# Performance work log

Measured on AMD Instinct MI355X. Metric: run time of the kernel, lower is better.

## Reference

```python
import jax, jax.numpy as jnp
import numpy as np

NEG_SLOPE = 0.2  # PyG GATConv default


def add_self_loops(edge_index, num_nodes):
    loops = jnp.arange(num_nodes, dtype=edge_index.dtype)
    return jnp.concatenate([edge_index, jnp.stack([loops, loops])], axis=1)


def gat_conv(x, edge_index, W, att_src, att_dst, bias, heads, out_ch, concat):
    # x: [N, F_in]; edge_index: [2, E] with row0=src(j), row1=dst(i)
    N = x.shape[0]
    xl = (x @ W).reshape(N, heads, out_ch)              # [N, H, C]
    src, dst = edge_index[0], edge_index[1]
    a_src = jnp.einsum('nhc,hc->nh', xl, att_src)        # [N, H]
    a_dst = jnp.einsum('nhc,hc->nh', xl, att_dst)        # [N, H]
    alpha = jax.nn.leaky_relu(a_src[src] + a_dst[dst], NEG_SLOPE)  # [E, H]
    # segment softmax over incoming edges of each dst node
    m = jax.ops.segment_max(alpha, dst, num_segments=N)  # [N, H]
    e = jnp.exp(alpha - m[dst])
    denom = jax.ops.segment_sum(e, dst, num_segments=N)
    coef = e / (denom[dst] + 1e-16)                      # [E, H]
    msg = xl[src] * coef[..., None]                      # [E, H, C]
    out = jax.ops.segment_sum(msg, dst, num_segments=N)  # [N, H, C]
    out = out.reshape(N, heads * out_ch) if concat else out.mean(axis=1)
    return out + bias


def setup_inputs() -> dict:
    key = jax.random.key(0)
    ks = jax.random.split(key, 12)
    N, E = 50000, 800000
    nfeat, nhid, nheads, nclass = 512, 8, 8, 16
    hid = nhid * nheads  # 64
    s1 = 1.0 / np.sqrt(nfeat)
    s2 = 1.0 / np.sqrt(hid)
    return {
        'x': jax.random.normal(ks[0], (N, nfeat), jnp.float32),
        'edge_index': jax.random.randint(ks[1], (2, E), 0, N, jnp.int64 if jax.config.jax_enable_x64 else jnp.int32),
        'W1': jax.random.uniform(ks[2], (nfeat, hid), jnp.float32, -s1, s1),
        'att_src1': jax.random.uniform(ks[3], (nheads, nhid), jnp.float32, -s2, s2),
        'att_dst1': jax.random.uniform(ks[4], (nheads, nhid), jnp.float32, -s2, s2),
        'bias1': jnp.zeros((hid,), jnp.float32),
        'W2': jax.random.uniform(ks[5], (hid, nclass), jnp.float32, -s2, s2),
        'att_src2': jax.random.uniform(ks[6], (1, nclass), jnp.float32, -0.25, 0.25),
        'att_dst2': jax.random.uniform(ks[7], (1, nclass), jnp.float32, -0.25, 0.25),
        'bias2': jnp.zeros((nclass,), jnp.float32),
    }


def reference(x, edge_index, W1, att_src1, att_dst1, bias1, W2, att_src2, att_dst2, bias2):
    N = x.shape[0]
    ei = add_self_loops(edge_index, N)
    # dropout layers are identity at inference
    h = gat_conv(x, ei, W1, att_src1, att_dst1, bias1, heads=8, out_ch=8, concat=True)
    o = gat_conv(h, ei, W2, att_src2, att_dst2, bias2, heads=1, out_ch=16, concat=True)
    o = jax.nn.elu(o)
    return jax.nn.log_softmax(o, axis=1)
```

## Files before the change

kernel.cpp:

```cpp
#include <hip/hip_runtime.h>
#include <hip/hip_bf16.h>
#include <math.h>

#define NEG_SLOPE 0.2f

typedef short short8 __attribute__((ext_vector_type(8)));
typedef float floatx4 __attribute__((ext_vector_type(4)));

static __device__ __forceinline__ float bf2f(unsigned short u) {
  return __uint_as_float(((unsigned int)u) << 16);
}
static __device__ __forceinline__ unsigned short f2bf(float f) {
  unsigned int u = __float_as_uint(f);
  u = (u + 0x7fffu + ((u >> 16) & 1u)) >> 16;
  return (unsigned short)u;
}
static __device__ __forceinline__ unsigned int pack2(float a, float b) {
  __hip_bfloat162 h = __float22bfloat162_rn(make_float2(a, b));
  unsigned int u;
  __builtin_memcpy(&u, &h, 4);
  return u;
}

__global__ void prep_kernel(const float* __restrict__ W1, unsigned short* __restrict__ W1t,
                            int* __restrict__ deg, const int* __restrict__ ei,
                            unsigned short* __restrict__ src16, unsigned short* __restrict__ dst16,
                            int N, int E) {
  int i = blockIdx.x * 256 + threadIdx.x;
  if (i < 32768) {
    int k = i >> 6, c = i & 63;
    W1t[c * 512 + k] = f2bf(W1[i]);
  }
  int j = i - 32768;
  if (j >= 0 && j < N) deg[j] = 1;
  int e = i - 32768 - N;
  if (e >= 0 && e < E) {
    src16[e] = (unsigned short)ei[e];
    dst16[e] = (unsigned short)ei[E + e];
  }
}

__global__ __launch_bounds__(256) void gemm1_mfma(const float* __restrict__ A,
                                                  const unsigned short* __restrict__ W1t,
                                                  const float* __restrict__ att_src,
                                                  const float* __restrict__ att_dst,
                                                  unsigned short* __restrict__ xlb,
                                                  float* __restrict__ a_src,
                                                  float* __restrict__ a_dst, int M) {
  __shared__ unsigned short As[64 * 72];
  __shared__ unsigned short Bs[64 * 72];
  int tid = threadIdx.x;
  int w = tid >> 6, lane = tid & 63;
  int q = lane >> 4, cl = lane & 15;
  int row0 = blockIdx.x << 6;
  floatx4 acc[4] = {};

  int sr = tid >> 2;
  int skq = (tid & 3) << 4;
  int arow = row0 + sr;
  const float* Aptr = A + (size_t)arow * 512 + skq;
  const unsigned short* Bptr = W1t + sr * 512 + skq;
  unsigned short* AsW = As + sr * 72 + skq;
  unsigned short* BsW = Bs + sr * 72 + skq;

  for (int k0 = 0; k0 < 512; k0 += 64) {
    float4 f0 = make_float4(0.f, 0.f, 0.f, 0.f), f1 = f0, f2 = f0, f3 = f0;
    if (arow < M) {
      f0 = *(const float4*)(Aptr + k0);
      f1 = *(const float4*)(Aptr + k0 + 4);
      f2 = *(const float4*)(Aptr + k0 + 8);
      f3 = *(const float4*)(Aptr + k0 + 12);
    }
    uint4 b0 = *(const uint4*)(Bptr + k0);
    uint4 b1 = *(const uint4*)(Bptr + k0 + 8);
    __syncthreads();
    uint4 a0, a1;
    a0.x = pack2(f0.x, f0.y); a0.y = pack2(f0.z, f0.w);
    a0.z = pack2(f1.x, f1.y); a0.w = pack2(f1.z, f1.w);
    a1.x = pack2(f2.x, f2.y); a1.y = pack2(f2.z, f2.w);
    a1.z = pack2(f3.x, f3.y); a1.w = pack2(f3.z, f3.w);
    *(uint4*)(AsW) = a0;
    *(uint4*)(AsW + 8) = a1;
    *(uint4*)(BsW) = b0;
    *(uint4*)(BsW + 8) = b1;
    __syncthreads();
#pragma unroll
    for (int kk = 0; kk < 2; ++kk) {
      short8 af = *(const short8*)(As + (w * 16 + cl) * 72 + kk * 32 + q * 8);
#pragma unroll
      for (int t = 0; t < 4; ++t) {
        short8 bf = *(const short8*)(Bs + (t * 16 + cl) * 72 + kk * 32 + q * 8);
        acc[t] = __builtin_amdgcn_mfma_f32_16x16x32_bf16(af, bf, acc[t], 0, 0, 0);
      }
    }
  }

  float asv[4], adv[4];
#pragma unroll
  for (int t = 0; t < 4; ++t) {
    asv[t] = att_src[t * 16 + cl];
    adv[t] = att_dst[t * 16 + cl];
  }
#pragma unroll
  for (int reg = 0; reg < 4; ++reg) {
    int r = row0 + w * 16 + q * 4 + reg;
    bool ok = r < M;
#pragma unroll
    for (int t = 0; t < 4; ++t) {
      float v = acc[t][reg];
      if (ok) xlb[(size_t)r * 64 + t * 16 + cl] = f2bf(v);
      float ps = v * asv[t];
      float pd = v * adv[t];
      ps += __shfl_xor(ps, 1); pd += __shfl_xor(pd, 1);
      ps += __shfl_xor(ps, 2); pd += __shfl_xor(pd, 2);
      ps += __shfl_xor(ps, 4); pd += __shfl_xor(pd, 4);
      if (ok && (cl & 7) == 0) {
        int h = t * 2 + (cl >> 3);
        a_src[r * 8 + h] = ps;
        a_dst[r * 8 + h] = pd;
      }
    }
  }
}

__global__ __launch_bounds__(256) void deg_hist_sliced(const unsigned short* __restrict__ dst16,
                                                       int* __restrict__ deg,
                                                       int E, int N, int ipc) {
  int slice = blockIdx.x & 7;
  int chunk = blockIdx.x >> 3;
  int lo = (int)(((long long)slice * N) >> 3);
  int hi = (int)(((long long)(slice + 1) * N) >> 3);
  int beg = chunk * ipc;
  int end = min(beg + ipc, E);
  for (int i = beg + threadIdx.x; i < end; i += 256) {
    int d = dst16[i];
    if (d >= lo && d < hi) atomicAdd(&deg[d], 1);
  }
}

__global__ __launch_bounds__(256) void partial_sums(const int* __restrict__ deg,
                                                    int* __restrict__ partials, int N) {
  __shared__ int ws[4];
  int base = blockIdx.x * 512;
  int tid = threadIdx.x;
  int i0 = base + tid * 2;
  int s = 0;
  if (i0 < N) s += deg[i0];
  if (i0 + 1 < N) s += deg[i0 + 1];
#pragma unroll
  for (int off = 32; off >= 1; off >>= 1) s += __shfl_xor(s, off, 64);
  if ((tid & 63) == 0) ws[tid >> 6] = s;
  __syncthreads();
  if (tid == 0) partials[blockIdx.x] = ws[0] + ws[1] + ws[2] + ws[3];
}

__global__ __launch_bounds__(256) void scan_partials(const int* __restrict__ partials,
                                                     int* __restrict__ blockoff,
                                                     int* __restrict__ rowptr, int nb, int N) {
  __shared__ int sums[256];
  int tid = threadIdx.x;
  int chunk = (nb + 255) >> 8;
  int start = tid * chunk, end = min(start + chunk, nb);
  int s = 0;
  for (int i = start; i < end; ++i) s += partials[i];
  sums[tid] = s;
  __syncthreads();
  for (int off = 1; off < 256; off <<= 1) {
    int t = (tid >= off) ? sums[tid - off] : 0;
    __syncthreads();
    sums[tid] += t;
    __syncthreads();
  }
  int run = (tid == 0) ? 0 : sums[tid - 1];
  for (int i = start; i < end; ++i) {
    blockoff[i] = run;
    run += partials[i];
  }
  if (tid == 255) rowptr[N] = sums[255];
}

__global__ __launch_bounds__(256) void scan_blocks(const int* __restrict__ deg,
                                                   const int* __restrict__ blockoff,
                                                   int* __restrict__ rowptr,
                                                   int* __restrict__ cursor, int N) {
  __shared__ int wavesum[4];
  int base = blockIdx.x * 512;
  int tid = threadIdx.x;
  int lane = tid & 63, wv = tid >> 6;
  int i0 = base + tid * 2;
  int d0 = (i0 < N) ? deg[i0] : 0;
  int d1 = (i0 + 1 < N) ? deg[i0 + 1] : 0;
  int s = d0 + d1;
  int v = s;
#pragma unroll
  for (int off = 1; off < 64; off <<= 1) {
    int t = __shfl_up(v, off, 64);
    if (lane >= off) v += t;
  }
  if (lane == 63) wavesum[wv] = v;
  __syncthreads();
  int woff = 0;
  for (int w = 0; w < wv; ++w) woff += wavesum[w];
  int excl = v - s + woff + blockoff[blockIdx.x];
  if (i0 < N) { rowptr[i0] = excl; cursor[i0] = excl; }
  if (i0 + 1 < N) { rowptr[i0 + 1] = excl + d0; cursor[i0 + 1] = excl + d0; }
}

__global__ __launch_bounds__(256) void scatter_sliced(const unsigned short* __restrict__ src16,
                                                      const unsigned short* __restrict__ dst16,
                                                      int* __restrict__ cursor,
                                                      unsigned short* __restrict__ srcs,
                                                      int E, int N, int ipc) {
  int slice = blockIdx.x & 7;
  int chunk = blockIdx.x >> 3;
  int lo = (int)(((long long)slice * N) >> 3);
  int hi = (int)(((long long)(slice + 1) * N) >> 3);
  int total = E + N;
  int beg = chunk * ipc;
  int end = min(beg + ipc, total);
  for (int i = beg + threadIdx.x; i < end; i += 256) {
    int d = (i < E) ? (int)dst16[i] : (i - E);
    if (d >= lo && d < hi) {
      int s = (i < E) ? (int)src16[i] : d;
      int pos = atomicAdd(&cursor[d], 1);
      srcs[pos] = (unsigned short)s;
    }
  }
}

__global__ __launch_bounds__(256) void agg1_csr(const int* __restrict__ rowptr,
                                                const unsigned short* __restrict__ srcs,
                                                const float* __restrict__ a_src,
                                                const float* __restrict__ a_dst,
                                                const unsigned short* __restrict__ xlb,
                                                float* __restrict__ agg1, int N) {
  int wave = (blockIdx.x * blockDim.x + threadIdx.x) >> 6;
  int lane = threadIdx.x & 63;
  if (wave >= N) return;
  int h = lane >> 3;
  int beg = rowptr[wave], end = rowptr[wave + 1];
  float ad = a_dst[wave * 8 + h];
  float den = 0.f, acc = 0.f;
  int p = beg;
  for (; p + 8 <= end; p += 8) {
    int myv = (int)srcs[p + (lane & 7)];
    int s0 = __builtin_amdgcn_readlane(myv, 0);
    int s1 = __builtin_amdgcn_readlane(myv, 1);
    int s2 = __builtin_amdgcn_readlane(myv, 2);
    int s3 = __builtin_amdgcn_readlane(myv, 3);
    int s4 = __builtin_amdgcn_readlane(myv, 4);
    int s5 = __builtin_amdgcn_readlane(myv, 5);
    int s6 = __builtin_amdgcn_readlane(myv, 6);
    int s7 = __builtin_amdgcn_readlane(myv, 7);
    float a0 = a_src[s0 * 8 + h], a1 = a_src[s1 * 8 + h];
    float a2 = a_src[s2 * 8 + h], a3 = a_src[s3 * 8 + h];
    float a4 = a_src[s4 * 8 + h], a5 = a_src[s5 * 8 + h];
    float a6 = a_src[s6 * 8 + h], a7 = a_src[s7 * 8 + h];
    float x0 = bf2f(xlb[(size_t)s0 * 64 + lane]);
    float x1 = bf2f(xlb[(size_t)s1 * 64 + lane]);
    float x2 = bf2f(xlb[(size_t)s2 * 64 + lane]);
    float x3 = bf2f(xlb[(size_t)s3 * 64 + lane]);
    float x4 = bf2f(xlb[(size_t)s4 * 64 + lane]);
    float x5 = bf2f(xlb[(size_t)s5 * 64 + lane]);
    float x6 = bf2f(xlb[(size_t)s6 * 64 + lane]);
    float x7 = bf2f(xlb[(size_t)s7 * 64 + lane]);
    a0 += ad; a1 += ad; a2 += ad; a3 += ad;
    a4 += ad; a5 += ad; a6 += ad; a7 += ad;
    a0 = a0 >= 0.f ? a0 : NEG_SLOPE * a0;
    a1 = a1 >= 0.f ? a1 : NEG_SLOPE * a1;
    a2 = a2 >= 0.f ? a2 : NEG_SLOPE * a2;
    a3 = a3 >= 0.f ? a3 : NEG_SLOPE * a3;
    a4 = a4 >= 0.f ? a4 : NEG_SLOPE * a4;
    a5 = a5 >= 0.f ? a5 : NEG_SLOPE * a5;
    a6 = a6 >= 0.f ? a6 : NEG_SLOPE * a6;
    a7 = a7 >= 0.f ? a7 : NEG_SLOPE * a7;
    float w0 = __expf(a0), w1 = __expf(a1), w2 = __expf(a2), w3 = __expf(a3);
    float w4 = __expf(a4), w5 = __expf(a5), w6 = __expf(a6), w7 = __expf(a7);
    den += ((w0 + w1) + (w2 + w3)) + ((w4 + w5) + (w6 + w7));
    acc += w0 * x0 + w1 * x1 + w2 * x2 + w3 * x3;
    acc += w4 * x4 + w5 * x5 + w6 * x6 + w7 * x7;
  }
  for (; p < end; ++p) {
    int s = __builtin_amdgcn_readfirstlane((int)srcs[p]);
    float a = a_src[s * 8 + h] + ad;
    a = a >= 0.f ? a : NEG_SLOPE * a;
    float w = __expf(a);
    den += w;
    acc += w * bf2f(xlb[(size_t)s * 64 + lane]);
  }
  agg1[(size_t)wave * 64 + lane] = acc / (den + 1e-16f);
}

__global__ __launch_bounds__(256) void gemm2_prep(const float* __restrict__ agg1,
                                                  const float* __restrict__ bias1,
                                                  const float* __restrict__ W2,
                                                  const float* __restrict__ att_src2,
                                                  const float* __restrict__ att_dst2,
                                                  float* __restrict__ xl2,
                                                  float* __restrict__ a_src2,
                                                  float* __restrict__ a_dst2, int N) {
  __shared__ float hs[16 * 68];
  int tid = threadIdx.x;
  int n0 = blockIdx.x << 4;
  {
    int node = tid >> 4;
    int off = (tid & 15) << 2;
    int nn = n0 + node;
    float4 v = make_float4(0.f, 0.f, 0.f, 0.f);
    if (nn < N) {
      v = *(const float4*)(agg1 + (size_t)nn * 64 + off);
      float4 b = *(const float4*)(bias1 + off);
      v.x += b.x; v.y += b.y; v.z += b.z; v.w += b.w;
    }
    *(float4*)(hs + node * 68 + off) = v;
  }
  __syncthreads();
  int t = tid >> 4, c = tid & 15;
  int n = n0 + t;
  if (n >= N) return;
  float sum = 0.f;
#pragma unroll
  for (int k = 0; k < 64; ++k) sum += hs[t * 68 + k] * W2[k * 16 + c];
  xl2[(size_t)n * 16 + c] = sum;
  float ps = sum * att_src2[c];
  float pd = sum * att_dst2[c];
#pragma unroll
  for (int w = 8; w >= 1; w >>= 1) {
    ps += __shfl_xor(ps, w, 16);
    pd += __shfl_xor(pd, w, 16);
  }
  if (c == 0) {
    a_src2[n] = ps;
    a_dst2[n] = pd;
  }
}

__global__ __launch_bounds__(256) void agg2_fin(const int* __restrict__ rowptr,
                                                const unsigned short* __restrict__ srcs,
                                                const float* __restrict__ a_src2,
                                                const float* __restrict__ a_dst2,
                                                const float* __restrict__ xl2,
                                                const float* __restrict__ bias2,
                                                float* __restrict__ out, int N) {
  int t = blockIdx.x * blockDim.x + threadIdx.x;
  int node = t >> 4;
  int c = t & 15;
  if (node >= N) return;
  int beg = rowptr[node], end = rowptr[node + 1];
  float ad = a_dst2[node];
  float den = 0.f, acc = 0.f;
  int p = beg;
  for (; p + 8 <= end; p += 8) {
    int s0 = srcs[p], s1 = srcs[p + 1], s2 = srcs[p + 2], s3 = srcs[p + 3];
    int s4 = srcs[p + 4], s5 = srcs[p + 5], s6 = srcs[p + 6], s7 = srcs[p + 7];
    float a0 = a_src2[s0], a1 = a_src2[s1], a2 = a_src2[s2], a3 = a_src2[s3];
    float a4 = a_src2[s4], a5 = a_src2[s5], a6 = a_src2[s6], a7 = a_src2[s7];
    float x0 = xl2[(size_t)s0 * 16 + c], x1 = xl2[(size_t)s1 * 16 + c];
    float x2 = xl2[(size_t)s2 * 16 + c], x3 = xl2[(size_t)s3 * 16 + c];
    float x4 = xl2[(size_t)s4 * 16 + c], x5 = xl2[(size_t)s5 * 16 + c];
    float x6 = xl2[(size_t)s6 * 16 + c], x7 = xl2[(size_t)s7 * 16 + c];
    a0 += ad; a1 += ad; a2 += ad; a3 += ad;
    a4 += ad; a5 += ad; a6 += ad; a7 += ad;
    a0 = a0 >= 0.f ? a0 : NEG_SLOPE * a0;
    a1 = a1 >= 0.f ? a1 : NEG_SLOPE * a1;
    a2 = a2 >= 0.f ? a2 : NEG_SLOPE * a2;
    a3 = a3 >= 0.f ? a3 : NEG_SLOPE * a3;
    a4 = a4 >= 0.f ? a4 : NEG_SLOPE * a4;
    a5 = a5 >= 0.f ? a5 : NEG_SLOPE * a5;
    a6 = a6 >= 0.f ? a6 : NEG_SLOPE * a6;
    a7 = a7 >= 0.f ? a7 : NEG_SLOPE * a7;
    float w0 = __expf(a0), w1 = __expf(a1), w2 = __expf(a2), w3 = __expf(a3);
    float w4 = __expf(a4), w5 = __expf(a5), w6 = __expf(a6), w7 = __expf(a7);
    den += ((w0 + w1) + (w2 + w3)) + ((w4 + w5) + (w6 + w7));
    acc += w0 * x0 + w1 * x1 + w2 * x2 + w3 * x3;
    acc += w4 * x4 + w5 * x5 + w6 * x6 + w7 * x7;
  }
  for (; p < end; ++p) {
    int s = srcs[p];
    float a = a_src2[s] + ad;
    a = a >= 0.f ? a : NEG_SLOPE * a;
    float w = __expf(a);
    den += w;
    acc += w * xl2[(size_t)s * 16 + c];
  }
  float o = acc / (den + 1e-16f) + bias2[c];
  o = o > 0.f ? o : expm1f(o);
  float mx = o;
#pragma unroll
  for (int w = 8; w >= 1; w >>= 1) mx = fmaxf(mx, __shfl_xor(mx, w, 16));
  float e = __expf(o - mx);
  float ssum = e;
#pragma unroll
  for (int w = 8; w >= 1; w >>= 1) ssum += __shfl_xor(ssum, w, 16);
  out[(size_t)node * 16 + c] = o - mx - logf(ssum);
}

extern "C" void kernel_launch(void* const* d_in, const int* in_sizes, int n_in,
                              void* d_out, int out_size, void* d_ws, size_t ws_size,
                              hipStream_t stream) {
  const float* x        = (const float*)d_in[0];
  const int*   ei       = (const int*)d_in[1];
  const float* W1       = (const float*)d_in[2];
  const float* att_src1 = (const float*)d_in[3];
  const float* att_dst1 = (const float*)d_in[4];
  const float* bias1    = (const float*)d_in[5];
  const float* W2       = (const float*)d_in[6];
  const float* att_src2 = (const float*)d_in[7];
  const float* att_dst2 = (const float*)d_in[8];
  const float* bias2    = (const float*)d_in[9];
  float* out = (float*)d_out;

  int N = in_sizes[0] / 512;
  int E = in_sizes[1] / 2;
  int nb = (N + 511) / 512;

  char* wsp = (char*)d_ws;
  auto alloc = [&](size_t bytes) {
    char* p = wsp;
    wsp += (bytes + 255) & ~(size_t)255;
    return p;
  };
  unsigned short* xlb   = (unsigned short*)alloc((size_t)N * 64 * 2);
  unsigned short* W1t   = (unsigned short*)alloc((size_t)512 * 64 * 2);
  float* a_src1 = (float*)alloc((size_t)N * 8 * 4);
  float* a_dst1 = (float*)alloc((size_t)N * 8 * 4);
  float* agg1   = (float*)alloc((size_t)N * 64 * 4);
  float* xl2    = (float*)alloc((size_t)N * 16 * 4);
  float* a_src2 = (float*)alloc((size_t)N * 4);
  float* a_dst2 = (float*)alloc((size_t)N * 4);
  int* deg      = (int*)alloc((size_t)N * 4);
  int* rowptr   = (int*)alloc((size_t)(N + 1) * 4);
  int* cursor   = (int*)alloc((size_t)N * 4);
  int* partials = (int*)alloc((size_t)nb * 4);
  int* blockoff = (int*)alloc((size_t)nb * 4);
  unsigned short* src16 = (unsigned short*)alloc((size_t)E * 2);
  unsigned short* dst16 = (unsigned short*)alloc((size_t)E * 2);
  unsigned short* srcs  = (unsigned short*)alloc((size_t)(E + N) * 2);

  const int NCHUNK = 256;
  int ipc_h = (E + NCHUNK - 1) / NCHUNK;
  int ipc_s = (E + N + NCHUNK - 1) / NCHUNK;

  prep_kernel<<<(32768 + N + E + 255) / 256, 256, 0, stream>>>(W1, W1t, deg, ei, src16, dst16, N, E);
  deg_hist_sliced<<<NCHUNK * 8, 256, 0, stream>>>(dst16, deg, E, N, ipc_h);
  partial_sums<<<nb, 256, 0, stream>>>(deg, partials, N);
  scan_partials<<<1, 256, 0, stream>>>(partials, blockoff, rowptr, nb, N);
  scan_blocks<<<nb, 256, 0, stream>>>(deg, blockoff, rowptr, cursor, N);
  scatter_sliced<<<NCHUNK * 8, 256, 0, stream>>>(src16, dst16, cursor, srcs, E, N, ipc_s);

  gemm1_mfma<<<(N + 63) / 64, 256, 0, stream>>>(x, W1t, att_src1, att_dst1,
                                                xlb, a_src1, a_dst1, N);
  agg1_csr<<<((size_t)N * 64 + 255) / 256, 256, 0, stream>>>(rowptr, srcs, a_src1, a_dst1,
                                                             xlb, agg1, N);
  gemm2_prep<<<(N + 15) / 16, 256, 0, stream>>>(agg1, bias1, W2, att_src2, att_dst2,
                                                xl2, a_src2, a_dst2, N);
  agg2_fin<<<((size_t)N * 16 + 255) / 256, 256, 0, stream>>>(rowptr, srcs, a_src2, a_dst2,
                                                             xl2, bias2, out, N);
}
```

Before: 331.1 us.

## Fuse degree histogram into GEMM1 launch and use single-pass chained scan

The degree histogram blocks are merged into the GEMM1 kernel launch as extra leading blocks, so histogram atomics run concurrently with the MFMA GEMM. The three-kernel scan (partial sums, partial scan, block scan) is replaced by one decoupled-lookback chained scan using per-block flags, which prep_kernel zeroes. This removes several kernel launches and lets the latency-bound histogram overlap the GEMM. The lookback relies on earlier blocks being scheduled first to avoid spinning.

```diff
diff --git a/kernel.cpp b/kernel.cpp
--- a/kernel.cpp
+++ b/kernel.cpp
@@ -25,7 +25,7 @@
 __global__ void prep_kernel(const float* __restrict__ W1, unsigned short* __restrict__ W1t,
                             int* __restrict__ deg, const int* __restrict__ ei,
                             unsigned short* __restrict__ src16, unsigned short* __restrict__ dst16,
-                            int N, int E) {
+                            int* __restrict__ flags, int nb, int N, int E) {
   int i = blockIdx.x * 256 + threadIdx.x;
   if (i < 32768) {
     int k = i >> 6, c = i & 63;
@@ -38,23 +38,41 @@
     src16[e] = (unsigned short)ei[e];
     dst16[e] = (unsigned short)ei[E + e];
   }
-}
-
-__global__ __launch_bounds__(256) void gemm1_mfma(const float* __restrict__ A,
+  int f = i - 32768 - N - E;
+  if (f >= 0 && f < nb) flags[f] = 0;
+}
+
+__global__ __launch_bounds__(256) void hist_gemm1(const int* __restrict__ ei,
+                                                  int* __restrict__ deg,
+                                                  const float* __restrict__ A,
                                                   const unsigned short* __restrict__ W1t,
                                                   const float* __restrict__ att_src,
                                                   const float* __restrict__ att_dst,
                                                   unsigned short* __restrict__ xlb,
                                                   float* __restrict__ a_src,
-                                                  float* __restrict__ a_dst, int M) {
+                                                  float* __restrict__ a_dst,
+                                                  int M, int E, int N, int ipc, int HB) {
   __shared__ unsigned short As[64 * 72];
   __shared__ unsigned short Bs[64 * 72];
+  if (blockIdx.x < (unsigned)HB) {
+    int slice = blockIdx.x & 7;
+    int chunk = blockIdx.x >> 3;
+    int lo = (int)(((long long)slice * N) >> 3);
+    int hi = (int)(((long long)(slice + 1) * N) >> 3);
+    int beg = chunk * ipc;
+    int end = min(beg + ipc, E);
+    for (int i = beg + threadIdx.x; i < end; i += 256) {
+      int d = ei[E + i];
+      if (d >= lo && d < hi) atomicAdd(&deg[d], 1);
+    }
+    return;
+  }
   int tid = threadIdx.x;
   int w = tid >> 6, lane = tid & 63;
   int q = lane >> 4, cl = lane & 15;
-  int row0 = blockIdx.x << 6;
+  int row0 = (blockIdx.x - HB) << 6;
+
   floatx4 acc[4] = {};
-
   int sr = tid >> 2;
   int skq = (tid & 3) << 4;
   int arow = row0 + sr;
@@ -123,68 +141,17 @@
   }
 }
 
-__global__ __launch_bounds__(256) void deg_hist_sliced(const unsigned short* __restrict__ dst16,
-                                                       int* __restrict__ deg,
-                                                       int E, int N, int ipc) {
-  int slice = blockIdx.x & 7;
-  int chunk = blockIdx.x >> 3;
-  int lo = (int)(((long long)slice * N) >> 3);
-  int hi = (int)(((long long)(slice + 1) * N) >> 3);
-  int beg = chunk * ipc;
-  int end = min(beg + ipc, E);
-  for (int i = beg + threadIdx.x; i < end; i += 256) {
-    int d = dst16[i];
-    if (d >= lo && d < hi) atomicAdd(&deg[d], 1);
-  }
-}
-
-__global__ __launch_bounds__(256) void partial_sums(const int* __restrict__ deg,
-                                                    int* __restrict__ partials, int N) {
-  __shared__ int ws[4];
-  int base = blockIdx.x * 512;
-  int tid = threadIdx.x;
-  int i0 = base + tid * 2;
-  int s = 0;
-  if (i0 < N) s += deg[i0];
-  if (i0 + 1 < N) s += deg[i0 + 1];
-#pragma unroll
-  for (int off = 32; off >= 1; off >>= 1) s += __shfl_xor(s, off, 64);
-  if ((tid & 63) == 0) ws[tid >> 6] = s;
-  __syncthreads();
-  if (tid == 0) partials[blockIdx.x] = ws[0] + ws[1] + ws[2] + ws[3];
-}
-
-__global__ __launch_bounds__(256) void scan_partials(const int* __restrict__ partials,
-                                                     int* __restrict__ blockoff,
-                                                     int* __restrict__ rowptr, int nb, int N) {
-  __shared__ int sums[256];
-  int tid = threadIdx.x;
-  int chunk = (nb + 255) >> 8;
-  int start = tid * chunk, end = min(start + chunk, nb);
-  int s = 0;
-  for (int i = start; i < end; ++i) s += partials[i];
-  sums[tid] = s;
-  __syncthreads();
-  for (int off = 1; off < 256; off <<= 1) {
-    int t = (tid >= off) ? sums[tid - off] : 0;
-    __syncthreads();
-    sums[tid] += t;
-    __syncthreads();
-  }
-  int run = (tid == 0) ? 0 : sums[tid - 1];
-  for (int i = start; i < end; ++i) {
-    blockoff[i] = run;
-    run += partials[i];
-  }
-  if (tid == 255) rowptr[N] = sums[255];
-}
-
-__global__ __launch_bounds__(256) void scan_blocks(const int* __restrict__ deg,
-                                                   const int* __restrict__ blockoff,
-                                                   int* __restrict__ rowptr,
-                                                   int* __restrict__ cursor, int N) {
+__global__ __launch_bounds__(256) void scan_chained(const int* __restrict__ deg,
+                                                    int* __restrict__ rowptr,
+                                                    int* __restrict__ cursor,
+                                                    int* __restrict__ block_agg,
+                                                    int* __restrict__ block_pfx,
+                                                    int* __restrict__ flags,
+                                                    int N, int nb) {
   __shared__ int wavesum[4];
-  int base = blockIdx.x * 512;
+  __shared__ int base_sh;
+  int bid = blockIdx.x;
+  int base = bid * 512;
   int tid = threadIdx.x;
   int lane = tid & 63, wv = tid >> 6;
   int i0 = base + tid * 2;
@@ -199,9 +166,32 @@
   }
   if (lane == 63) wavesum[wv] = v;
   __syncthreads();
-  int woff = 0;
+  int S = wavesum[0] + wavesum[1] + wavesum[2] + wavesum[3];
+  if (tid == 0) {
+    if (bid == 0) {
+      block_pfx[0] = S;
+      __hip_atomic_store(&flags[0], 2, __ATOMIC_RELEASE, __HIP_MEMORY_SCOPE_AGENT);
+      base_sh = 0;
+      if (nb == 1) rowptr[N] = S;
+    } else {
+      block_agg[bid] = S;
+      __hip_atomic_store(&flags[bid], 1, __ATOMIC_RELEASE, __HIP_MEMORY_SCOPE_AGENT);
+      int run = 0, j = bid - 1;
+      while (true) {
+        int f = __hip_atomic_load(&flags[j], __ATOMIC_ACQUIRE, __HIP_MEMORY_SCOPE_AGENT);
+        if (f == 2) { run += block_pfx[j]; break; }
+        if (f == 1) { run += block_agg[j]; --j; }
+      }
+      block_pfx[bid] = run + S;
+      __hip_atomic_store(&flags[bid], 2, __ATOMIC_RELEASE, __HIP_MEMORY_SCOPE_AGENT);
+      base_sh = run;
+      if (bid == nb - 1) rowptr[N] = run + S;
+    }
+  }
+  __syncthreads();
+  int woff = base_sh;
   for (int w = 0; w < wv; ++w) woff += wavesum[w];
-  int excl = v - s + woff + blockoff[blockIdx.x];
+  int excl = v - s + woff;
   if (i0 < N) { rowptr[i0] = excl; cursor[i0] = excl; }
   if (i0 + 1 < N) { rowptr[i0 + 1] = excl + d0; cursor[i0 + 1] = excl + d0; }
 }
@@ -431,25 +421,25 @@
   int* deg      = (int*)alloc((size_t)N * 4);
   int* rowptr   = (int*)alloc((size_t)(N + 1) * 4);
   int* cursor   = (int*)alloc((size_t)N * 4);
-  int* partials = (int*)alloc((size_t)nb * 4);
-  int* blockoff = (int*)alloc((size_t)nb * 4);
+  int* block_agg = (int*)alloc((size_t)nb * 4);
+  int* block_pfx = (int*)alloc((size_t)nb * 4);
+  int* flags     = (int*)alloc((size_t)nb * 4);
   unsigned short* src16 = (unsigned short*)alloc((size_t)E * 2);
   unsigned short* dst16 = (unsigned short*)alloc((size_t)E * 2);
   unsigned short* srcs  = (unsigned short*)alloc((size_t)(E + N) * 2);
 
   const int NCHUNK = 256;
+  const int HB = NCHUNK * 8;
   int ipc_h = (E + NCHUNK - 1) / NCHUNK;
   int ipc_s = (E + N + NCHUNK - 1) / NCHUNK;
-
-  prep_kernel<<<(32768 + N + E + 255) / 256, 256, 0, stream>>>(W1, W1t, deg, ei, src16, dst16, N, E);
-  deg_hist_sliced<<<NCHUNK * 8, 256, 0, stream>>>(dst16, deg, E, N, ipc_h);
-  partial_sums<<<nb, 256, 0, stream>>>(deg, partials, N);
-  scan_partials<<<1, 256, 0, stream>>>(partials, blockoff, rowptr, nb, N);
-  scan_blocks<<<nb, 256, 0, stream>>>(deg, blockoff, rowptr, cursor, N);
+  int GB = (N + 63) / 64;
+
+  prep_kernel<<<(32768 + N + E + nb + 255) / 256, 256, 0, stream>>>(
+      W1, W1t, deg, ei, src16, dst16, flags, nb, N, E);
+  hist_gemm1<<<HB + GB, 256, 0, stream>>>(ei, deg, x, W1t, att_src1, att_dst1,
+                                          xlb, a_src1, a_dst1, N, E, N, ipc_h, HB);
+  scan_chained<<<nb, 256, 0, stream>>>(deg, rowptr, cursor, block_agg, block_pfx, flags, N, nb);
   scatter_sliced<<<NCHUNK * 8, 256, 0, stream>>>(src16, dst16, cursor, srcs, E, N, ipc_s);
-
-  gemm1_mfma<<<(N + 63) / 64, 256, 0, stream>>>(x, W1t, att_src1, att_dst1,
-                                                xlb, a_src1, a_dst1, N);
   agg1_csr<<<((size_t)N * 64 + 255) / 256, 256, 0, stream>>>(rowptr, srcs, a_src1, a_dst1,
                                                              xlb, agg1, N);
   gemm2_prep<<<(N + 15) / 16, 256, 0, stream>>>(agg1, bias1, W2, att_src2, att_dst2,
```

Result: slower. 344.3 us (+4.0%).
